# Kernel optimization log

Hardware: AMD Instinct MI355X
Metric: run time of the kernel (lower is better)

## Reference

```python
import jax, jax.numpy as jnp
import numpy as np

HEAD_DIM = 64
N_HEADS = 16
DIM = 1024
EPS = 1e-6
GRID = 32  # make_axial_pos(32, 32)


def _make_theta(head_dim=HEAD_DIM, n_heads=N_HEADS):
    hd8 = head_dim // 8
    nh2 = n_heads // 2
    freqs = np.exp(np.linspace(np.log(np.pi), np.log(10 * np.pi), hd8 * nh2 + 1)[:-1])
    freqs = freqs.reshape(hd8, nh2).T  # (nh2, hd8)
    # axial positions on a 32x32 grid, cell centers in [-1, 1]
    p = np.linspace(-1.0, 1.0, GRID + 1)
    p = (p[:-1] + p[1:]) / 2
    pos = np.stack(np.meshgrid(p, p, indexing='ij'), axis=-1).reshape(GRID * GRID, 2)
    pos = np.concatenate([np.zeros((1, 2)), pos], axis=0)  # (1025, 2)
    th1 = np.concatenate([pos[:-1, None, 0:1] * freqs, pos[:-1, None, 1:2] * freqs], axis=-1)
    th2 = np.concatenate([pos[1:, None, 0:1] * freqs, pos[1:, None, 1:2] * freqs], axis=-1)
    # (seq=1024, n_heads, head_dim//4)
    return np.concatenate([th1, th2], axis=1).astype(np.float32)


def setup_inputs() -> dict:
    key = jax.random.key(0)
    k1, k2, k3 = jax.random.split(key, 3)
    B, S = 8, 1024
    x = jax.random.normal(k1, (B, S, DIM), dtype=jnp.float32)
    scale = jnp.ones((DIM,), dtype=jnp.float32)
    w_qkv = jax.random.normal(k2, (3 * DIM, DIM), dtype=jnp.float32) * 0.02
    w_out = jax.random.normal(k3, (DIM, DIM), dtype=jnp.float32) * 0.02
    theta = jnp.asarray(_make_theta())
    return {"x": x, "scale": scale, "w_qkv": w_qkv, "w_out": w_out, "theta": theta}


def _rms_norm(x, scale, eps):
    xf = x.astype(jnp.float32)
    mean_sq = jnp.mean(xf * xf, axis=-1, keepdims=True)
    s = scale.astype(jnp.float32) * jax.lax.rsqrt(mean_sq + eps)
    return x * s.astype(x.dtype)


def _rope(x, theta):
    # x: (B, H, S, D); theta: (H, S, d) with d = D // 4 -> rotates first D//2 dims
    d = theta.shape[-1]
    cos = jnp.cos(theta)
    sin = jnp.sin(theta)
    x1, x2, rest = x[..., :d], x[..., d:2 * d], x[..., 2 * d:]
    y1 = x1 * cos - x2 * sin
    y2 = x2 * cos + x1 * sin
    return jnp.concatenate([y1, y2, rest], axis=-1)


def reference(x, scale, w_qkv, w_out, theta):
    B, S, dim = x.shape
    H = N_HEADS
    D = dim // H
    skip = x
    xn = _rms_norm(x, scale, EPS)
    qkv = xn @ w_qkv.T                                  # (B, S, 3*dim)
    qkv = qkv.reshape(B, S, 3, H, D).transpose(0, 3, 2, 1, 4)  # (B, H, 3, S, D)
    q, k, v = qkv[:, :, 0], qkv[:, :, 1], qkv[:, :, 2]  # (B, H, S, D)
    th = theta[:S].transpose(1, 0, 2)                   # (H, S, D//4)
    q = _rope(q, th)
    k = _rope(k, th)
    scores = jnp.einsum('bhsd,bhtd->bhst', q, k) / jnp.sqrt(jnp.float32(D))
    causal = jnp.tril(jnp.ones((S, S), dtype=bool))
    scores = jnp.where(causal, scores, jnp.finfo(scores.dtype).min)
    attn = jax.nn.softmax(scores, axis=-1)
    o = jnp.einsum('bhst,bhtd->bhsd', attn, v)          # (B, H, S, D)
    o = o.transpose(0, 2, 1, 3).reshape(B, S, dim)
    return o @ w_out.T + skip
```

## Files before the change

kernel.cpp:

```cpp
#include <hip/hip_runtime.h>
#include <hip/hip_bf16.h>
#include <cstdint>

typedef short short8 __attribute__((ext_vector_type(8)));
typedef float f32x4 __attribute__((ext_vector_type(4)));

#define MFMA16(a, b, c) __builtin_amdgcn_mfma_f32_16x16x32_bf16((a), (b), (c), 0, 0, 0)

__device__ __forceinline__ unsigned short f2b(float f) {
    __hip_bfloat16 h = __float2bfloat16(f);
    return __builtin_bit_cast(unsigned short, h);
}

__device__ __forceinline__ void gl_lds16(const void* g, void* l) {
    __builtin_amdgcn_global_load_lds((const __attribute__((address_space(1))) void*)g,
                                     (__attribute__((address_space(3))) void*)l, 16, 0, 0);
}

#define QSC 0.18033688011112042f

__global__ void rmsnorm_kernel(const float* __restrict__ x, const float* __restrict__ scale,
                               unsigned short* __restrict__ xn) {
    const int row = blockIdx.x;
    const int tid = threadIdx.x;
    const float4* xr = (const float4*)(x + (size_t)row * 1024);
    float4 vx = xr[tid];
    float ss = vx.x * vx.x + vx.y * vx.y + vx.z * vx.z + vx.w * vx.w;
#pragma unroll
    for (int m = 1; m < 64; m <<= 1) ss += __shfl_xor(ss, m);
    __shared__ float wsum[4];
    if ((tid & 63) == 0) wsum[tid >> 6] = ss;
    __syncthreads();
    float tot = wsum[0] + wsum[1] + wsum[2] + wsum[3];
    float rs = rsqrtf(tot * (1.0f / 1024.0f) + 1e-6f);
    const float4* sr = (const float4*)scale;
    float4 sv = sr[tid];
    ushort4 r;
    r.x = f2b(vx.x * sv.x * rs);
    r.y = f2b(vx.y * sv.y * rs);
    r.z = f2b(vx.z * sv.z * rs);
    r.w = f2b(vx.w * sv.w * rs);
    *(ushort4*)(xn + (size_t)row * 1024 + tid * 4) = r;
}

__global__ void f2b_kernel(const float* __restrict__ in, unsigned short* __restrict__ outp, int n4) {
    int i = blockIdx.x * 256 + threadIdx.x;
    if (i < n4) {
        float4 vv = ((const float4*)in)[i];
        ushort4 r;
        r.x = f2b(vv.x);
        r.y = f2b(vv.y);
        r.z = f2b(vv.z);
        r.w = f2b(vv.w);
        ((ushort4*)outp)[i] = r;
    }
}

constexpr int BM = 128, BN = 128, BK = 64, KDIM = 1024, NT = KDIM / BK;

template <int EPI>
__launch_bounds__(256, 4) __global__
    void gemm_bt(const unsigned short* __restrict__ A, const unsigned short* __restrict__ Bw,
                 unsigned short* __restrict__ qo, unsigned short* __restrict__ ko,
                 unsigned short* __restrict__ vo, const float* __restrict__ skip,
                 float* __restrict__ out, const float* __restrict__ theta) {
    __shared__ unsigned short As[BM * BK];
    __shared__ unsigned short Bs[BN * BK];
    const int tid = threadIdx.x;
    const int lane = tid & 63, w = tid >> 6;
    const int wr = w >> 1, wc = w & 1;
    const int lr = lane & 15, lg = lane >> 4;
    constexpr int NBX = (EPI == 0) ? 24 : 8;
    const int f = blockIdx.x;
    const int xcd = f & 7, wloc = f >> 3;
    const int g = xcd * (NBX * 8) + wloc;
    const int bx = g % NBX, by = g / NBX;
    const int m0 = by * BM;
    const int n0 = bx * BN;
    const int NCOL = (EPI == 0) ? 3072 : 1024;

    f32x4 acc[4][4] = {};

    auto stage = [&](int kt) {
        const int k0 = kt * BK;
#pragma unroll
        for (int i = 0; i < 4; ++i) {
            int seg = i * 256 + tid;
            int row = seg >> 3, c8 = (seg & 7) ^ (row & 7);
            gl_lds16(A + (size_t)(m0 + row) * KDIM + k0 + c8 * 8, &As[(i * 256 + w * 64) * 8]);
            gl_lds16(Bw + (size_t)(n0 + row) * KDIM + k0 + c8 * 8, &Bs[(i * 256 + w * 64) * 8]);
        }
    };

    for (int kt = 0; kt < NT; ++kt) {
        stage(kt);
        __syncthreads();
#pragma unroll
        for (int kkc = 0; kkc < 2; ++kkc) {
            short8 a[4], b[4];
            const int slot = ((kkc * 4 + lg) ^ (lr & 7)) * 8;
#pragma unroll
            for (int m = 0; m < 4; ++m)
                a[m] = *(const short8*)&As[(wr * 64 + m * 16 + lr) * BK + slot];
#pragma unroll
            for (int n = 0; n < 4; ++n)
                b[n] = *(const short8*)&Bs[(wc * 64 + n * 16 + lr) * BK + slot];
#pragma unroll
            for (int m = 0; m < 4; ++m)
#pragma unroll
                for (int n = 0; n < 4; ++n) acc[m][n] = MFMA16(a[m], b[n], acc[m][n]);
        }
        __syncthreads();
    }

    if (EPI == 0) {
        const int colb = n0 + wc * 64;
        const int c = colb >> 10, h = (colb >> 6) & 15;
#pragma unroll
        for (int m = 0; m < 4; ++m) {
            int grow0 = m0 + wr * 64 + m * 16 + lg * 4;
            int b = grow0 >> 10, s0 = grow0 & 1023;
            if (c == 2) {
#pragma unroll
                for (int n = 0; n < 4; ++n) {
                    int d = n * 16 + lr;
                    ushort4 r;
                    r.x = f2b(acc[m][n][0]);
                    r.y = f2b(acc[m][n][1]);
                    r.z = f2b(acc[m][n][2]);
                    r.w = f2b(acc[m][n][3]);
                    *(ushort4*)&vo[(((size_t)(b * 16 + h)) * 64 + d) * 1024 + s0] = r;
                }
            } else {
                unsigned short* dst = (c == 0) ? qo : ko;
                float sc = (c == 0) ? QSC : 1.0f;
#pragma unroll
                for (int j = 0; j < 4; ++j) {
                    int s = s0 + j;
                    float th = theta[((s * 16 + h) << 4) + lr];
                    float sn, cs;
                    __sincosf(th, &sn, &cs);
                    float x1 = acc[m][0][j], x2 = acc[m][1][j];
                    size_t rowb = (((size_t)(b * 16 + h)) * 1024 + s) * 64;
                    dst[rowb + lr]      = f2b((x1 * cs - x2 * sn) * sc);
                    dst[rowb + 16 + lr] = f2b((x2 * cs + x1 * sn) * sc);
                    dst[rowb + 32 + lr] = f2b(acc[m][2][j] * sc);
                    dst[rowb + 48 + lr] = f2b(acc[m][3][j] * sc);
                }
            }
        }
    } else {
#pragma unroll
        for (int m = 0; m < 4; ++m)
#pragma unroll
            for (int n = 0; n < 4; ++n) {
                int gcol = n0 + wc * 64 + n * 16 + lr;
#pragma unroll
                for (int j = 0; j < 4; ++j) {
                    int grow = m0 + wr * 64 + m * 16 + lg * 4 + j;
                    size_t idx = (size_t)grow * NCOL + gcol;
                    out[idx] = acc[m][n][j] + skip[idx];
                }
            }
    }
}

__launch_bounds__(256, 4) __global__
    void attn_kernel(const unsigned short* __restrict__ q, const unsigned short* __restrict__ k,
                     const unsigned short* __restrict__ vt, unsigned short* __restrict__ o) {
    constexpr int S = 1024, D = 64;
    __shared__ unsigned short KVs[4][4096];
    __shared__ unsigned Pls[4][16 * 32];
    const int tid = threadIdx.x, lane = tid & 63, w = tid >> 6;
    const int lr = lane & 15, lg = lane >> 4;
    const int f = blockIdx.x;
    constexpr int qmap[8] = {7, 6, 0, 1, 5, 4, 2, 3};
    const int qb = qmap[f >> 7];
    const int bh = (f & 7) * 16 + ((f >> 3) & 15);
    const int qs = qb * 128;
    const size_t base = (size_t)bh * (S * D);
    const int wrow0 = qs + w * 32;

    short8 qf[2][2];
#pragma unroll
    for (int m = 0; m < 2; ++m) {
        const unsigned short* qp = q + base + (size_t)(wrow0 + m * 16 + lr) * D;
        qf[m][0] = *(const short8*)(qp + lg * 8);
        qf[m][1] = *(const short8*)(qp + 32 + lg * 8);
    }

    f32x4 of[2][4] = {};
    float mrun[2] = {-1e30f, -1e30f};
    float lrun[2] = {0.f, 0.f};

    const int nkt = 2 * qb + 2;

    auto stageK = [&](int buf, int kt) {
#pragma unroll
        for (int i = 0; i < 2; ++i) {
            int seg = i * 256 + tid;
            int row = seg >> 3, c8 = (seg & 7) ^ (row & 7);
            gl_lds16(k + base + (size_t)(kt * 64 + row) * D + c8 * 8,
                     &KVs[buf][(i * 256 + w * 64) * 8]);
        }
    };
    auto stageV = [&](int buf, int kt) {
#pragma unroll
        for (int i = 0; i < 2; ++i) {
            int seg = i * 256 + tid;
            int row = seg >> 3, c8 = (seg & 7) ^ (row & 7);
            gl_lds16(vt + base + (size_t)row * S + kt * 64 + c8 * 8,
                     &KVs[2 + buf][(i * 256 + w * 64) * 8]);
        }
    };

    unsigned* Pw = &Pls[w][0];
    const int swz = (lr & 7) << 2;

    stageK(0, 0);
    stageV(0, 0);
    __syncthreads();

    for (int kt = 0; kt < nkt; ++kt) {
        const int b = kt & 1;
        if (kt + 1 < nkt) {
            stageK(b ^ 1, kt + 1);
            stageV(b ^ 1, kt + 1);
        }

        if (kt * 64 <= wrow0 + 31) {
            f32x4 sf[2][4] = {};
            __builtin_amdgcn_s_setprio(1);
#pragma unroll
            for (int n = 0; n < 4; ++n) {
                const int r = n * 16 + lr;
#pragma unroll
                for (int kkc = 0; kkc < 2; ++kkc) {
                    short8 kf =
                        *(const short8*)&KVs[b][r * 64 + (((kkc * 4 + lg) ^ (lr & 7)) * 8)];
#pragma unroll
                    for (int m = 0; m < 2; ++m) sf[m][n] = MFMA16(kf, qf[m][kkc], sf[m][n]);
                }
            }
            __builtin_amdgcn_s_setprio(0);

            if (kt * 64 + 63 > wrow0) {
#pragma unroll
                for (int m = 0; m < 2; ++m)
#pragma unroll
                    for (int n = 0; n < 4; ++n)
#pragma unroll
                        for (int j = 0; j < 4; ++j) {
                            int t = kt * 64 + 16 * n + lg * 4 + j;
                            int qr = wrow0 + m * 16 + lr;
                            if (t > qr) sf[m][n][j] = -1e30f;
                        }
            }

#pragma unroll
            for (int m = 0; m < 2; ++m) {
                float mx = -1e30f;
#pragma unroll
                for (int n = 0; n < 4; ++n)
                    mx = fmaxf(mx, fmaxf(fmaxf(sf[m][n][0], sf[m][n][1]),
                                         fmaxf(sf[m][n][2], sf[m][n][3])));
                mx = fmaxf(mx, __shfl_xor(mx, 16));
                mx = fmaxf(mx, __shfl_xor(mx, 32));

                if (__any(mx > mrun[m] + 8.0f)) {
                    float newm = fmaxf(mrun[m], mx);
                    float sc = __builtin_amdgcn_exp2f(mrun[m] - newm);
                    mrun[m] = newm;
                    float psum = 0.f;
#pragma unroll
                    for (int n = 0; n < 4; ++n)
#pragma unroll
                        for (int j = 0; j < 4; ++j) {
                            float p = __builtin_amdgcn_exp2f(sf[m][n][j] - newm);
                            sf[m][n][j] = p;
                            psum += p;
                        }
                    lrun[m] = lrun[m] * sc + psum;
#pragma unroll
                    for (int n2 = 0; n2 < 4; ++n2) of[m][n2] *= sc;
                } else {
                    float mo = mrun[m];
                    float psum = 0.f;
#pragma unroll
                    for (int n = 0; n < 4; ++n)
#pragma unroll
                        for (int j = 0; j < 4; ++j) {
                            float p = __builtin_amdgcn_exp2f(sf[m][n][j] - mo);
                            sf[m][n][j] = p;
                            psum += p;
                        }
                    lrun[m] += psum;
                }
            }

            short8 pa[2][2];
#pragma unroll
            for (int m = 0; m < 2; ++m) {
                unsigned Dk[4][2];
#pragma unroll
                for (int n = 0; n < 4; ++n)
#pragma unroll
                    for (int w2 = 0; w2 < 2; ++w2)
                        Dk[n][w2] = (unsigned)f2b(sf[m][n][2 * w2]) |
                                    ((unsigned)f2b(sf[m][n][2 * w2 + 1]) << 16);
#pragma unroll
                for (int n = 0; n < 4; ++n)
#pragma unroll
                    for (int w2 = 0; w2 < 2; ++w2)
                        Pw[lr * 32 + ((8 * n + 2 * lg + w2) ^ swz)] = Dk[n][w2];
#pragma unroll
                for (int kkc = 0; kkc < 2; ++kkc)
                    pa[m][kkc] = *(const short8*)&Pw[lr * 32 + ((kkc * 16 + 4 * lg) ^ swz)];
            }

            __builtin_amdgcn_s_setprio(1);
#pragma unroll
            for (int kkc = 0; kkc < 2; ++kkc) {
#pragma unroll
                for (int n2 = 0; n2 < 4; ++n2) {
                    const int r = n2 * 16 + lr;
                    short8 bv =
                        *(const short8*)&KVs[2 + b][r * 64 + (((kkc * 4 + lg) ^ (lr & 7)) * 8)];
#pragma unroll
                    for (int m = 0; m < 2; ++m) of[m][n2] = MFMA16(pa[m][kkc], bv, of[m][n2]);
                }
            }
            __builtin_amdgcn_s_setprio(0);
        }

        __syncthreads();
    }

    float* Lw = (float*)&Pls[w][0];
#pragma unroll
    for (int m = 0; m < 2; ++m) {
        float l = lrun[m];
        l += __shfl_xor(l, 16);
        l += __shfl_xor(l, 32);
        Lw[m * 16 + lr] = l;
    }

    unsigned short* Ts = &KVs[0][0] + w * 2304;
    const int bb = bh >> 4, h = bh & 15;
#pragma unroll
    for (int m = 0; m < 2; ++m)
#pragma unroll
        for (int j = 0; j < 4; ++j) {
            float inv = 1.f / Lw[m * 16 + lg * 4 + j];
            int row = m * 16 + lg * 4 + j;
#pragma unroll
            for (int n2 = 0; n2 < 4; ++n2)
                Ts[row * 72 + n2 * 16 + lr] = f2b(of[m][n2][j] * inv);
        }
#pragma unroll
    for (int i = 0; i < 4; ++i) {
        int row = i * 8 + lg * 2 + (lr >> 3);
        short8 v = *(const short8*)&Ts[row * 72 + (lr & 7) * 8];
        size_t ob = ((size_t)(bb * 1024 + wrow0 + row)) * 1024 + h * 64 + (lr & 7) * 8;
        *(short8*)&o[ob] = v;
    }
}

extern "C" void kernel_launch(void* const* d_in, const int* in_sizes, int n_in, void* d_out,
                              int out_size, void* d_ws, size_t ws_size, hipStream_t stream) {
    const float* x = (const float*)d_in[0];
    const float* scale = (const float*)d_in[1];
    const float* w_qkv = (const float*)d_in[2];
    const float* w_out = (const float*)d_in[3];
    const float* theta = (const float*)d_in[4];
    float* out = (float*)d_out;

    char* p = (char*)d_ws;
    unsigned short* xn = (unsigned short*)p;      p += (size_t)8192 * 1024 * 2;
    unsigned short* wqb = (unsigned short*)p;     p += (size_t)3072 * 1024 * 2;
    unsigned short* wob = (unsigned short*)p;     p += (size_t)1024 * 1024 * 2;
    unsigned short* qb_ = (unsigned short*)p;     p += (size_t)128 * 1024 * 64 * 2;
    unsigned short* kb_ = (unsigned short*)p;     p += (size_t)128 * 1024 * 64 * 2;
    unsigned short* vb_ = (unsigned short*)p;     p += (size_t)128 * 1024 * 64 * 2;
    unsigned short* ob_ = (unsigned short*)p;     p += (size_t)8192 * 1024 * 2;

    rmsnorm_kernel<<<8192, 256, 0, stream>>>(x, scale, xn);
    f2b_kernel<<<3072, 256, 0, stream>>>(w_qkv, wqb, 786432);
    f2b_kernel<<<1024, 256, 0, stream>>>(w_out, wob, 262144);
    gemm_bt<0><<<1536, 256, 0, stream>>>(xn, wqb, qb_, kb_, vb_, nullptr, nullptr, theta);
    attn_kernel<<<1024, 256, 0, stream>>>(qb_, kb_, vb_, ob_);
    gemm_bt<1><<<512, 256, 0, stream>>>(ob_, wob, nullptr, nullptr, nullptr, x, out, nullptr);
}
```

Before: 164.9 us.

## Load K/V fragments directly from global memory in smaller attention blocks

Drops the LDS double-buffered K/V staging and block-wide barriers. Each wave now reads its K and V^T MFMA fragments straight from global memory (relying on L2/cache reuse). Blocks shrink to two waves, grid doubles, and per-wave work is ordered by descending row group for load balance. Only the last tile of each wave is masked. This removes sync overhead and LDS pressure but gives up shared reuse of K/V across waves, adding global/cache traffic.

```diff
diff --git a/kernel.cpp b/kernel.cpp
--- a/kernel.cpp
+++ b/kernel.cpp
@@ -165,21 +165,21 @@
     }
 }
 
-__launch_bounds__(256, 4) __global__
+__launch_bounds__(128, 4) __global__
     void attn_kernel(const unsigned short* __restrict__ q, const unsigned short* __restrict__ k,
                      const unsigned short* __restrict__ vt, unsigned short* __restrict__ o) {
     constexpr int S = 1024, D = 64;
-    __shared__ unsigned short KVs[4][4096];
-    __shared__ unsigned Pls[4][16 * 32];
-    const int tid = threadIdx.x, lane = tid & 63, w = tid >> 6;
+    __shared__ unsigned Pls[2][16 * 32];
+    __shared__ unsigned short Ts[2][32 * 72];
+    const int tid = threadIdx.x, lane = tid & 63, wv = tid >> 6;
     const int lr = lane & 15, lg = lane >> 4;
     const int f = blockIdx.x;
-    constexpr int qmap[8] = {7, 6, 0, 1, 5, 4, 2, 3};
-    const int qb = qmap[f >> 7];
     const int bh = (f & 7) * 16 + ((f >> 3) & 15);
-    const int qs = qb * 128;
+    const int pairi = f >> 7;
+    const int g = 31 - (pairi * 2 + wv);
+    const int wrow0 = g * 32;
     const size_t base = (size_t)bh * (S * D);
-    const int wrow0 = qs + w * 32;
+    const int nkt = (g >> 1) + 1;
 
     short8 qf[2][2];
 #pragma unroll
@@ -193,150 +193,117 @@
     float mrun[2] = {-1e30f, -1e30f};
     float lrun[2] = {0.f, 0.f};
 
-    const int nkt = 2 * qb + 2;
-
-    auto stageK = [&](int buf, int kt) {
-#pragma unroll
-        for (int i = 0; i < 2; ++i) {
-            int seg = i * 256 + tid;
-            int row = seg >> 3, c8 = (seg & 7) ^ (row & 7);
-            gl_lds16(k + base + (size_t)(kt * 64 + row) * D + c8 * 8,
-                     &KVs[buf][(i * 256 + w * 64) * 8]);
-        }
-    };
-    auto stageV = [&](int buf, int kt) {
-#pragma unroll
-        for (int i = 0; i < 2; ++i) {
-            int seg = i * 256 + tid;
-            int row = seg >> 3, c8 = (seg & 7) ^ (row & 7);
-            gl_lds16(vt + base + (size_t)row * S + kt * 64 + c8 * 8,
-                     &KVs[2 + buf][(i * 256 + w * 64) * 8]);
-        }
-    };
-
-    unsigned* Pw = &Pls[w][0];
+    unsigned* Pw = &Pls[wv][0];
     const int swz = (lr & 7) << 2;
 
-    stageK(0, 0);
-    stageV(0, 0);
-    __syncthreads();
-
     for (int kt = 0; kt < nkt; ++kt) {
-        const int b = kt & 1;
-        if (kt + 1 < nkt) {
-            stageK(b ^ 1, kt + 1);
-            stageV(b ^ 1, kt + 1);
-        }
-
-        if (kt * 64 <= wrow0 + 31) {
-            f32x4 sf[2][4] = {};
-            __builtin_amdgcn_s_setprio(1);
-#pragma unroll
-            for (int n = 0; n < 4; ++n) {
-                const int r = n * 16 + lr;
-#pragma unroll
-                for (int kkc = 0; kkc < 2; ++kkc) {
-                    short8 kf =
-                        *(const short8*)&KVs[b][r * 64 + (((kkc * 4 + lg) ^ (lr & 7)) * 8)];
-#pragma unroll
-                    for (int m = 0; m < 2; ++m) sf[m][n] = MFMA16(kf, qf[m][kkc], sf[m][n]);
-                }
-            }
-            __builtin_amdgcn_s_setprio(0);
-
-            if (kt * 64 + 63 > wrow0) {
-#pragma unroll
-                for (int m = 0; m < 2; ++m)
-#pragma unroll
-                    for (int n = 0; n < 4; ++n)
-#pragma unroll
-                        for (int j = 0; j < 4; ++j) {
-                            int t = kt * 64 + 16 * n + lg * 4 + j;
-                            int qr = wrow0 + m * 16 + lr;
-                            if (t > qr) sf[m][n][j] = -1e30f;
-                        }
-            }
-
+        const unsigned short* kb = k + base + (size_t)kt * 64 * D + lg * 8;
+        f32x4 sf[2][4] = {};
+        __builtin_amdgcn_s_setprio(1);
+#pragma unroll
+        for (int n = 0; n < 4; ++n) {
+            const unsigned short* kr = kb + (n * 16 + lr) * D;
+            short8 kf0 = *(const short8*)(kr);
+            short8 kf1 = *(const short8*)(kr + 32);
 #pragma unroll
             for (int m = 0; m < 2; ++m) {
-                float mx = -1e30f;
+                sf[m][n] = MFMA16(kf0, qf[m][0], sf[m][n]);
+                sf[m][n] = MFMA16(kf1, qf[m][1], sf[m][n]);
+            }
+        }
+        __builtin_amdgcn_s_setprio(0);
+
+        if (kt == nkt - 1) {
+#pragma unroll
+            for (int m = 0; m < 2; ++m)
 #pragma unroll
                 for (int n = 0; n < 4; ++n)
-                    mx = fmaxf(mx, fmaxf(fmaxf(sf[m][n][0], sf[m][n][1]),
-                                         fmaxf(sf[m][n][2], sf[m][n][3])));
-                mx = fmaxf(mx, __shfl_xor(mx, 16));
-                mx = fmaxf(mx, __shfl_xor(mx, 32));
-
-                if (__any(mx > mrun[m] + 8.0f)) {
-                    float newm = fmaxf(mrun[m], mx);
-                    float sc = __builtin_amdgcn_exp2f(mrun[m] - newm);
-                    mrun[m] = newm;
-                    float psum = 0.f;
-#pragma unroll
-                    for (int n = 0; n < 4; ++n)
-#pragma unroll
-                        for (int j = 0; j < 4; ++j) {
-                            float p = __builtin_amdgcn_exp2f(sf[m][n][j] - newm);
-                            sf[m][n][j] = p;
-                            psum += p;
-                        }
-                    lrun[m] = lrun[m] * sc + psum;
-#pragma unroll
-                    for (int n2 = 0; n2 < 4; ++n2) of[m][n2] *= sc;
-                } else {
-                    float mo = mrun[m];
-                    float psum = 0.f;
-#pragma unroll
-                    for (int n = 0; n < 4; ++n)
-#pragma unroll
-                        for (int j = 0; j < 4; ++j) {
-                            float p = __builtin_amdgcn_exp2f(sf[m][n][j] - mo);
-                            sf[m][n][j] = p;
-                            psum += p;
-                        }
-                    lrun[m] += psum;
-                }
-            }
-
-            short8 pa[2][2];
+#pragma unroll
+                    for (int j = 0; j < 4; ++j) {
+                        int t = kt * 64 + 16 * n + lg * 4 + j;
+                        int qr = wrow0 + m * 16 + lr;
+                        if (t > qr) sf[m][n][j] = -1e30f;
+                    }
+        }
+
+#pragma unroll
+        for (int m = 0; m < 2; ++m) {
+            float mx = -1e30f;
+#pragma unroll
+            for (int n = 0; n < 4; ++n)
+                mx = fmaxf(mx, fmaxf(fmaxf(sf[m][n][0], sf[m][n][1]),
+                                     fmaxf(sf[m][n][2], sf[m][n][3])));
+            mx = fmaxf(mx, __shfl_xor(mx, 16));
+            mx = fmaxf(mx, __shfl_xor(mx, 32));
+
+            if (__any(mx > mrun[m] + 8.0f)) {
+                float newm = fmaxf(mrun[m], mx);
+                float sc = __builtin_amdgcn_exp2f(mrun[m] - newm);
+                mrun[m] = newm;
+                float psum = 0.f;
+#pragma unroll
+                for (int n = 0; n < 4; ++n)
+#pragma unroll
+                    for (int j = 0; j < 4; ++j) {
+                        float p = __builtin_amdgcn_exp2f(sf[m][n][j] - newm);
+                        sf[m][n][j] = p;
+                        psum += p;
+                    }
+                lrun[m] = lrun[m] * sc + psum;
+#pragma unroll
+                for (int n2 = 0; n2 < 4; ++n2) of[m][n2] *= sc;
+            } else {
+                float mo = mrun[m];
+                float psum = 0.f;
+#pragma unroll
+                for (int n = 0; n < 4; ++n)
+#pragma unroll
+                    for (int j = 0; j < 4; ++j) {
+                        float p = __builtin_amdgcn_exp2f(sf[m][n][j] - mo);
+                        sf[m][n][j] = p;
+                        psum += p;
+                    }
+                lrun[m] += psum;
+            }
+        }
+
+        short8 pa[2][2];
+#pragma unroll
+        for (int m = 0; m < 2; ++m) {
+            unsigned Dk[4][2];
+#pragma unroll
+            for (int n = 0; n < 4; ++n)
+#pragma unroll
+                for (int w2 = 0; w2 < 2; ++w2)
+                    Dk[n][w2] = (unsigned)f2b(sf[m][n][2 * w2]) |
+                                ((unsigned)f2b(sf[m][n][2 * w2 + 1]) << 16);
+#pragma unroll
+            for (int n = 0; n < 4; ++n)
+#pragma unroll
+                for (int w2 = 0; w2 < 2; ++w2)
+                    Pw[lr * 32 + ((8 * n + 2 * lg + w2) ^ swz)] = Dk[n][w2];
+#pragma unroll
+            for (int kkc = 0; kkc < 2; ++kkc)
+                pa[m][kkc] = *(const short8*)&Pw[lr * 32 + ((kkc * 16 + 4 * lg) ^ swz)];
+        }
+
+        const unsigned short* vb = vt + base + kt * 64 + lg * 8;
+        __builtin_amdgcn_s_setprio(1);
+#pragma unroll
+        for (int n2 = 0; n2 < 4; ++n2) {
+            const unsigned short* vr = vb + (size_t)(n2 * 16 + lr) * S;
+            short8 bv0 = *(const short8*)(vr);
+            short8 bv1 = *(const short8*)(vr + 32);
 #pragma unroll
             for (int m = 0; m < 2; ++m) {
-                unsigned Dk[4][2];
-#pragma unroll
-                for (int n = 0; n < 4; ++n)
-#pragma unroll
-                    for (int w2 = 0; w2 < 2; ++w2)
-                        Dk[n][w2] = (unsigned)f2b(sf[m][n][2 * w2]) |
-                                    ((unsigned)f2b(sf[m][n][2 * w2 + 1]) << 16);
-#pragma unroll
-                for (int n = 0; n < 4; ++n)
-#pragma unroll
-                    for (int w2 = 0; w2 < 2; ++w2)
-                        Pw[lr * 32 + ((8 * n + 2 * lg + w2) ^ swz)] = Dk[n][w2];
-#pragma unroll
-                for (int kkc = 0; kkc < 2; ++kkc)
-                    pa[m][kkc] = *(const short8*)&Pw[lr * 32 + ((kkc * 16 + 4 * lg) ^ swz)];
-            }
-
-            __builtin_amdgcn_s_setprio(1);
-#pragma unroll
-            for (int kkc = 0; kkc < 2; ++kkc) {
-#pragma unroll
-                for (int n2 = 0; n2 < 4; ++n2) {
-                    const int r = n2 * 16 + lr;
-                    short8 bv =
-                        *(const short8*)&KVs[2 + b][r * 64 + (((kkc * 4 + lg) ^ (lr & 7)) * 8)];
-#pragma unroll
-                    for (int m = 0; m < 2; ++m) of[m][n2] = MFMA16(pa[m][kkc], bv, of[m][n2]);
-                }
-            }
-            __builtin_amdgcn_s_setprio(0);
-        }
-
-        __syncthreads();
-    }
-
-    float* Lw = (float*)&Pls[w][0];
+                of[m][n2] = MFMA16(pa[m][0], bv0, of[m][n2]);
+                of[m][n2] = MFMA16(pa[m][1], bv1, of[m][n2]);
+            }
+        }
+        __builtin_amdgcn_s_setprio(0);
+    }
+
+    float* Lw = (float*)&Pls[wv][0];
 #pragma unroll
     for (int m = 0; m < 2; ++m) {
         float l = lrun[m];
@@ -345,7 +312,7 @@
         Lw[m * 16 + lr] = l;
     }
 
-    unsigned short* Ts = &KVs[0][0] + w * 2304;
+    unsigned short* Tw = &Ts[wv][0];
     const int bb = bh >> 4, h = bh & 15;
 #pragma unroll
     for (int m = 0; m < 2; ++m)
@@ -355,12 +322,12 @@
             int row = m * 16 + lg * 4 + j;
 #pragma unroll
             for (int n2 = 0; n2 < 4; ++n2)
-                Ts[row * 72 + n2 * 16 + lr] = f2b(of[m][n2][j] * inv);
+                Tw[row * 72 + n2 * 16 + lr] = f2b(of[m][n2][j] * inv);
         }
 #pragma unroll
     for (int i = 0; i < 4; ++i) {
         int row = i * 8 + lg * 2 + (lr >> 3);
-        short8 v = *(const short8*)&Ts[row * 72 + (lr & 7) * 8];
+        short8 v = *(const short8*)&Tw[row * 72 + (lr & 7) * 8];
         size_t ob = ((size_t)(bb * 1024 + wrow0 + row)) * 1024 + h * 64 + (lr & 7) * 8;
         *(short8*)&o[ob] = v;
     }
@@ -388,6 +355,6 @@
     f2b_kernel<<<3072, 256, 0, stream>>>(w_qkv, wqb, 786432);
     f2b_kernel<<<1024, 256, 0, stream>>>(w_out, wob, 262144);
     gemm_bt<0><<<1536, 256, 0, stream>>>(xn, wqb, qb_, kb_, vb_, nullptr, nullptr, theta);
-    attn_kernel<<<1024, 256, 0, stream>>>(qb_, kb_, vb_, ob_);
+    attn_kernel<<<2048, 128, 0, stream>>>(qb_, kb_, vb_, ob_);
     gemm_bt<1><<<512, 256, 0, stream>>>(ob_, wob, nullptr, nullptr, nullptr, x, out, nullptr);
 }
```

After: 186.2 us. 12.9% more time.
